# Performance work log

Hardware: AMD Instinct MI355X
Metric: run time of the kernel (lower is better)

## Reference

```python
import jax, jax.numpy as jnp
import numpy as np

EPS = 1e-5
GROUPS = 32
HEADS = 8
RES_SCALE = 0.7071067811865476  # 1/sqrt(2)


def group_norm(x, groups, weight=None, bias=None):
    # x: [b, c, t]; normalize over (c//groups, t) per group, like torch GroupNorm
    b, c, t = x.shape
    xg = x.reshape(b, groups, (c // groups) * t)
    mean = xg.mean(axis=-1, keepdims=True)
    var = xg.var(axis=-1, keepdims=True)
    xg = (xg - mean) * jax.lax.rsqrt(var + EPS)
    x = xg.reshape(b, c, t)
    if weight is not None:
        x = x * weight[None, :, None] + bias[None, :, None]
    return x


def setup_inputs() -> dict:
    key = jax.random.key(0)
    ks = jax.random.split(key, 7)
    b, c, hh, ww = 8, 512, 32, 32
    return {
        "x": jax.random.normal(ks[0], (b, c, hh, ww), dtype=jnp.float32),
        "gn_w": jax.random.uniform(ks[1], (c,), dtype=jnp.float32, minval=0.5, maxval=1.5),
        "gn_b": jax.random.normal(ks[2], (c,), dtype=jnp.float32) * 0.1,
        "qkv_w": jax.random.normal(ks[3], (3 * c, c), dtype=jnp.float32) * (c ** -0.5),
        "qkv_b": jax.random.normal(ks[4], (3 * c,), dtype=jnp.float32) * 0.02,
        "proj_w": jax.random.normal(ks[5], (c, c), dtype=jnp.float32) * 0.02,
        "proj_b": jax.random.normal(ks[6], (c,), dtype=jnp.float32) * 0.02,
    }


def reference(x, gn_w, gn_b, qkv_w, qkv_b, proj_w, proj_b):
    b, c, hh, ww = x.shape
    t = hh * ww
    ch = c // HEADS
    xf = x.reshape(b, c, t)
    xn = group_norm(xf, GROUPS, gn_w, gn_b)
    # 1x1 conv -> GEMM: [b, 3c, t]
    qkv = jnp.einsum('oc,bct->bot', qkv_w, xn) + qkv_b[None, :, None]
    # split order: per head contiguous [q_ch; k_ch; v_ch]
    qkv = qkv.reshape(b * HEADS, 3 * ch, t)
    q, k, v = jnp.split(qkv, 3, axis=1)
    scale = ch ** -0.25
    w = jnp.einsum('bct,bcs->bts', q * scale, k * scale)
    w = jax.nn.softmax(w.astype(jnp.float32), axis=-1).astype(qkv.dtype)
    a = jnp.einsum('bts,bcs->bct', w, v).reshape(b, c, t)
    h = jnp.einsum('oc,bct->bot', proj_w, a) + proj_b[None, :, None]
    out = group_norm(RES_SCALE * xn + h, GROUPS)  # functional group_norm: no affine
    return out.reshape(b, c, hh, ww)
```

## Files before the change

### kernel.cpp

```cpp
#include <hip/hip_runtime.h>


typedef unsigned short u16;
typedef __attribute__((ext_vector_type(8))) short short8v;
typedef __attribute__((ext_vector_type(4))) float float4v;

constexpr int NB = 8, NC = 512, NT = 1024, CPG = 16;
#define EPSV 1e-5f
#define RES_SCALE 0.7071067811865476f
#define QK_SCALE 0.35355339059327376f
#define LOG2E 1.4426950408889634f

static __device__ __forceinline__ u16 f2bf(float f) {
  unsigned int u = __builtin_bit_cast(unsigned int, f);
  u = (u + 0x7fffu + ((u >> 16) & 1u)) >> 16;
  return (u16)u;
}
static __device__ __forceinline__ float exp2_fast(float x) {
  float r;
  asm("v_exp_f32 %0, %1" : "=v"(r) : "v"(x));
  return r;
}

template<bool AFFINE>
__global__ __launch_bounds__(256) void groupnorm_kernel(
    const float* __restrict__ src0, const float* __restrict__ gw,
    const float* __restrict__ gb, float* __restrict__ dst0)
{
  const int tid = threadIdx.x;
  const int b = blockIdx.x >> 5;
  const int g = blockIdx.x & 31;
  const size_t off = ((size_t)(b * NC + g * CPG)) * NT;
  const float* src = src0 + off;
  float* dst = dst0 + off;

  const float4* s4 = (const float4*)src;
  float sum = 0.f, sq = 0.f;
  #pragma unroll 4
  for (int i = tid; i < CPG * NT / 4; i += 256) {
    float4 v = s4[i];
    sum += v.x + v.y + v.z + v.w;
    sq  += v.x * v.x + v.y * v.y + v.z * v.z + v.w * v.w;
  }
  #pragma unroll
  for (int off2 = 32; off2; off2 >>= 1) {
    sum += __shfl_xor(sum, off2);
    sq  += __shfl_xor(sq,  off2);
  }
  __shared__ float rs[4], rq[4], stats[2];
  const int wave = tid >> 6, lane = tid & 63;
  if (lane == 0) { rs[wave] = sum; rq[wave] = sq; }
  __syncthreads();
  if (tid == 0) {
    float S = rs[0] + rs[1] + rs[2] + rs[3];
    float Q = rq[0] + rq[1] + rq[2] + rq[3];
    float mean = S * (1.0f / (CPG * NT));
    float var  = Q * (1.0f / (CPG * NT)) - mean * mean;
    stats[0] = mean;
    stats[1] = rsqrtf(var + EPSV);
  }
  __syncthreads();
  const float mean = stats[0], rstd = stats[1];
  float4* d4 = (float4*)dst;
  #pragma unroll 4
  for (int i = tid; i < CPG * NT / 4; i += 256) {
    float a, c2;
    if (AFFINE) {
      int ch = g * CPG + (i >> 8);
      float wv = gw[ch];
      a  = rstd * wv;
      c2 = gb[ch] - mean * a;
    } else {
      a  = rstd;
      c2 = -mean * rstd;
    }
    float4 v = s4[i];
    v.x = v.x * a + c2; v.y = v.y * a + c2;
    v.z = v.z * a + c2; v.w = v.w * a + c2;
    d4[i] = v;
  }
}

__global__ __launch_bounds__(256) void prep_kernel(
    const float* __restrict__ xnf, u16* __restrict__ xbt,
    const float* __restrict__ qw, const float* __restrict__ pw,
    u16* __restrict__ qwb, u16* __restrict__ pwb)
{
  __shared__ __attribute__((aligned(16))) u16 T[64 * 80];
  const int x = blockIdx.x;
  const int tid = threadIdx.x;
  if (x >= 1024) {
    const int i = (x - 1024) * 256 + tid;
    const float* in; u16* out; int j;
    if (i < 98304) { in = qw; out = qwb; j = i; }
    else           { in = pw; out = pwb; j = i - 98304; }
    const float4 a = *(const float4*)(in + (size_t)j * 8);
    const float4 b = *(const float4*)(in + (size_t)j * 8 + 4);
    short8v o;
    o[0] = (short)f2bf(a.x); o[1] = (short)f2bf(a.y);
    o[2] = (short)f2bf(a.z); o[3] = (short)f2bf(a.w);
    o[4] = (short)f2bf(b.x); o[5] = (short)f2bf(b.y);
    o[6] = (short)f2bf(b.z); o[7] = (short)f2bf(b.w);
    *(short8v*)(out + (size_t)j * 8) = o;
    return;
  }
  const int tt = x & 15, cc = (x >> 4) & 7, b = x >> 7;
  const int c = tid >> 2, tch = (tid & 3) * 16;
  const float* src = xnf + ((size_t)b * NC + cc * 64 + c) * NT + tt * 64 + tch;
  #pragma unroll
  for (int j = 0; j < 4; j++) {
    float4 v = *(const float4*)(src + j * 4);
    T[(tch + j * 4 + 0) * 80 + c] = f2bf(v.x);
    T[(tch + j * 4 + 1) * 80 + c] = f2bf(v.y);
    T[(tch + j * 4 + 2) * 80 + c] = f2bf(v.z);
    T[(tch + j * 4 + 3) * 80 + c] = f2bf(v.w);
  }
  __syncthreads();
  const int t = tid >> 2, cp = (tid & 3) * 2;
  u16* dst = xbt + ((size_t)b * NT + tt * 64 + t) * NC + cc * 64;
  #pragma unroll
  for (int q = 0; q < 2; q++)
    *(short8v*)(dst + (cp + q) * 8) = *(const short8v*)(T + t * 80 + (cp + q) * 8);
}

template<int MODE>
__global__ __launch_bounds__(256) void mfma_gemm_kernel(
    const u16* __restrict__ Wb, const float* __restrict__ bias,
    const u16* __restrict__ Bt, u16* __restrict__ qkT,
    u16* __restrict__ vN, float* __restrict__ outF,
    const float* __restrict__ xnf)
{
  __shared__ __attribute__((aligned(16))) u16 lds[(MODE == 1) ? 17408 : 16384];
  const int tid = threadIdx.x;
  const int w = tid >> 6, l = tid & 63, lr = l & 15, lg = l >> 4;
  const int wm = (w >> 1) * 64, wn = (w & 1) * 64;
  const int bn = blockIdx.x * 128, bm = blockIdx.y * 128, b = blockIdx.z;

  const u16* Ag = Wb + (size_t)bm * 512;
  const u16* Bg = Bt + ((size_t)b * NT + bn) * 512;

  const int srow = w * 16 + (l >> 2);
  const int scg  = (l & 3) ^ ((l >> 3) & 3);
  const u16* ap0 = Ag + (size_t)srow * 512 + scg * 8;
  const u16* bp0 = Bg + (size_t)srow * 512 + scg * 8;
  char* ldsb = (char*)lds;
  char* adst0 = ldsb + w * 1024;

  float4v acc[4][4];
  #pragma unroll
  for (int i = 0; i < 4; i++)
    #pragma unroll
    for (int j = 0; j < 4; j++) acc[i][j] = (float4v){0.f, 0.f, 0.f, 0.f};

  #pragma unroll
  for (int r = 0; r < 2; r++) {
    __builtin_amdgcn_global_load_lds(ap0 + r * 64 * 512, adst0 + r * 4096, 16, 0, 0);
    __builtin_amdgcn_global_load_lds(bp0 + r * 64 * 512, adst0 + 8192 + r * 4096, 16, 0, 0);
  }
  asm volatile("s_waitcnt vmcnt(0)" ::: "memory");
  __builtin_amdgcn_s_barrier();

  for (int ks = 0; ks < 16; ++ks) {
    const int buf = ks & 1;
    if (ks < 15) {
      const size_t k0n = (size_t)(ks + 1) * 32;
      char* an = ldsb + (buf ^ 1) * 16384 + w * 1024;
      #pragma unroll
      for (int r = 0; r < 2; r++) {
        __builtin_amdgcn_global_load_lds(ap0 + k0n + r * 64 * 512, an + r * 4096, 16, 0, 0);
        __builtin_amdgcn_global_load_lds(bp0 + k0n + r * 64 * 512, an + 8192 + r * 4096, 16, 0, 0);
      }
    }
    const u16* au = lds + buf * 8192;
    const u16* bu = au + 4096;
    short8v af[4], bf[4];
    #pragma unroll
    for (int mi = 0; mi < 4; mi++) {
      const int m = wm + mi * 16 + lr;
      af[mi] = *(const short8v*)(au + m * 32 + ((lg ^ ((m >> 1) & 3)) * 8));
    }
    #pragma unroll
    for (int ni = 0; ni < 4; ni++) {
      const int n = wn + ni * 16 + lr;
      bf[ni] = *(const short8v*)(bu + n * 32 + ((lg ^ ((n >> 1) & 3)) * 8));
    }
    #pragma unroll
    for (int mi = 0; mi < 4; mi++)
      #pragma unroll
      for (int ni = 0; ni < 4; ni++)
        acc[mi][ni] = __builtin_amdgcn_mfma_f32_16x16x32_bf16(af[mi], bf[ni], acc[mi][ni], 0, 0, 0);
    if (ks < 15) {
      asm volatile("s_waitcnt vmcnt(0)" ::: "memory");
      __builtin_amdgcn_s_barrier();
    }
  }

  if (MODE == 0) {
    #pragma unroll
    for (int mi = 0; mi < 4; mi++) {
      const int m0 = bm + wm + mi * 16 + lg * 4;
      const int head = m0 / 192;
      const int r0 = m0 - head * 192;
      const float4 bv4 = *(const float4*)(bias + m0);
      if (r0 < 128) {
        const float scl = (r0 < 64) ? QK_SCALE * LOG2E : QK_SCALE;
        const int col = head * 128 + r0;
        #pragma unroll
        for (int ni = 0; ni < 4; ni++) {
          const int t = bn + wn + ni * 16 + lr;
          unsigned int lo = (unsigned)f2bf((acc[mi][ni][0] + bv4.x) * scl) |
                            ((unsigned)f2bf((acc[mi][ni][1] + bv4.y) * scl) << 16);
          unsigned int hi = (unsigned)f2bf((acc[mi][ni][2] + bv4.z) * scl) |
                            ((unsigned)f2bf((acc[mi][ni][3] + bv4.w) * scl) << 16);
          *(uint2*)(qkT + ((size_t)b * NT + t) * 1024 + col) = make_uint2(lo, hi);
        }
      } else {
        const int vc = head * 64 + (r0 - 128);
        #pragma unroll
        for (int ni = 0; ni < 4; ni++) {
          const int t = bn + wn + ni * 16 + lr;
          vN[((size_t)b * NC + vc + 0) * NT + t] = f2bf(acc[mi][ni][0] + bv4.x);
          vN[((size_t)b * NC + vc + 1) * NT + t] = f2bf(acc[mi][ni][1] + bv4.y);
          vN[((size_t)b * NC + vc + 2) * NT + t] = f2bf(acc[mi][ni][2] + bv4.z);
          vN[((size_t)b * NC + vc + 3) * NT + t] = f2bf(acc[mi][ni][3] + bv4.w);
        }
      }
    }
  } else {
    float* Cs = (float*)lds;
    for (int ph = 0; ph < 2; ph++) {
      __syncthreads();
      if ((w >> 1) == ph) {
        #pragma unroll
        for (int mi = 0; mi < 4; mi++)
          #pragma unroll
          for (int ni = 0; ni < 4; ni++) {
            const int rr = mi * 16 + lg * 4;
            const int cc2 = wn + ni * 16 + lr;
            #pragma unroll
            for (int r = 0; r < 4; r++)
              Cs[(rr + r) * 136 + cc2] = acc[mi][ni][r];
          }
      }
      __syncthreads();
      const int mloc = tid >> 2;
      const int m = bm + ph * 64 + mloc;
      const float bv = bias[m];
      const int cb = (tid & 3) * 32;
      const float* cr = Cs + mloc * 136 + cb;
      const float* xr = xnf + ((size_t)b * NC + m) * NT + bn + cb;
      float* yr = outF + ((size_t)b * NC + m) * NT + bn + cb;
      #pragma unroll
      for (int j = 0; j < 8; j++) {
        float4 c4 = *(const float4*)(cr + j * 4);
        float4 x4 = *(const float4*)(xr + j * 4);
        float4 o;
        o.x = c4.x + bv + RES_SCALE * x4.x;
        o.y = c4.y + bv + RES_SCALE * x4.y;
        o.z = c4.z + bv + RES_SCALE * x4.z;
        o.w = c4.w + bv + RES_SCALE * x4.w;
        *(float4*)(yr + j * 4) = o;
      }
    }
  }
}

__global__ __launch_bounds__(256, 4) void attn_mfma_kernel(
    const u16* __restrict__ qkT, const u16* __restrict__ vN, u16* __restrict__ aT)
{
  __shared__ __attribute__((aligned(16))) u16 lds[5 * 4096];
  const int tid = threadIdx.x;
  const int w = tid >> 6, l = tid & 63, lr = l & 15, lg = l >> 4;
  const int L = blockIdx.x;
  const int bh = (L & 7) * 8 + ((L >> 3) & 7);
  const int t0 = (L >> 6) * 64;
  const int b = bh >> 3, h = bh & 7;

  const u16* qbase = qkT + (size_t)b * NT * 1024 + h * 128;
  const u16* kbase = qbase + 64;
  const u16* vbase = vN + ((size_t)b * NC + h * 64) * NT;

  const size_t qrow = (size_t)(t0 + w * 16 + lr) * 1024;
  const short8v qa0 = *(const short8v*)(qbase + qrow + lg * 8);
  const short8v qa1 = *(const short8v*)(qbase + qrow + 32 + lg * 8);

  const int strow = w * 8 + (l >> 3);
  const int scg = (l & 7) ^ (l >> 3);
  const u16* kp0 = kbase + (size_t)strow * 1024 + scg * 8;
  const u16* vp0 = vbase + (size_t)strow * 1024 + scg * 8;
  char* ldsb = (char*)lds;
  u16* Ps = lds + 16384;

  float4v out[4];
  #pragma unroll
  for (int nc = 0; nc < 4; nc++) out[nc] = (float4v){0.f, 0.f, 0.f, 0.f};
  float ps[4] = {0.f, 0.f, 0.f, 0.f};

  #pragma unroll
  for (int r = 0; r < 2; r++) {
    __builtin_amdgcn_global_load_lds(kp0 + (size_t)r * 32 * 1024,
                                     ldsb + w * 1024 + r * 4096, 16, 0, 0);
    __builtin_amdgcn_global_load_lds(vp0 + (size_t)r * 32 * 1024,
                                     ldsb + 16384 + w * 1024 + r * 4096, 16, 0, 0);
  }
  asm volatile("s_waitcnt vmcnt(0)" ::: "memory");
  __builtin_amdgcn_s_barrier();

  for (int it = 0; it < 16; ++it) {
    const int buf = it & 1;
    if (it < 15) {
      const size_t s0n = (size_t)(it + 1) * 64;
      char* kd = ldsb + (buf ^ 1) * 8192 + w * 1024;
      char* vd = ldsb + 16384 + (buf ^ 1) * 8192 + w * 1024;
      #pragma unroll
      for (int r = 0; r < 2; r++) {
        __builtin_amdgcn_global_load_lds(kp0 + (s0n + r * 32) * 1024, kd + r * 4096, 16, 0, 0);
        __builtin_amdgcn_global_load_lds(vp0 + s0n + (size_t)r * 32 * 1024, vd + r * 4096, 16, 0, 0);
      }
    }
    const u16* Kc = lds + buf * 4096;
    const u16* Vc = lds + 8192 + buf * 4096;

    float4v sacc[4];
    #pragma unroll
    for (int n = 0; n < 4; n++) sacc[n] = (float4v){0.f, 0.f, 0.f, 0.f};
    __builtin_amdgcn_s_setprio(1);
    #pragma unroll
    for (int n = 0; n < 4; n++) {
      const int srow = n * 16 + lr;
      short8v kb0 = *(const short8v*)(Kc + srow * 64 + ((lg ^ (srow & 7)) * 8));
      short8v kb1 = *(const short8v*)(Kc + srow * 64 + (((4 + lg) ^ (srow & 7)) * 8));
      sacc[n] = __builtin_amdgcn_mfma_f32_16x16x32_bf16(qa0, kb0, sacc[n], 0, 0, 0);
      sacc[n] = __builtin_amdgcn_mfma_f32_16x16x32_bf16(qa1, kb1, sacc[n], 0, 0, 0);
    }
    __builtin_amdgcn_s_setprio(0);

    #pragma unroll
    for (int n = 0; n < 4; n++) {
      #pragma unroll
      for (int r = 0; r < 4; r++) {
        float p = exp2_fast(sacc[n][r]);
        ps[r] += p;
        const int t = w * 16 + lg * 4 + r;
        Ps[t * 64 + ((n * 16 + lr) ^ ((t & 7) << 3))] =
            (u16)(__builtin_bit_cast(unsigned int, p) >> 16);
      }
    }

    __builtin_amdgcn_s_setprio(1);
    #pragma unroll
    for (int kc = 0; kc < 2; kc++) {
      const int prow = w * 16 + lr;
      short8v pa = *(const short8v*)(Ps + prow * 64 + ((kc * 32 + lg * 8) ^ ((prow & 7) << 3)));
      #pragma unroll
      for (int nc = 0; nc < 4; nc++) {
        const int crow = nc * 16 + lr;
        short8v vb = *(const short8v*)(Vc + crow * 64 + (((kc * 4 + lg) ^ (crow & 7)) * 8));
        out[nc] = __builtin_amdgcn_mfma_f32_16x16x32_bf16(pa, vb, out[nc], 0, 0, 0);
      }
    }
    __builtin_amdgcn_s_setprio(0);

    if (it < 15) {
      asm volatile("s_waitcnt vmcnt(0)" ::: "memory");
      __builtin_amdgcn_s_barrier();
    }
  }

  #pragma unroll
  for (int r = 0; r < 4; r++) {
    ps[r] += __shfl_xor(ps[r], 1);
    ps[r] += __shfl_xor(ps[r], 2);
    ps[r] += __shfl_xor(ps[r], 4);
    ps[r] += __shfl_xor(ps[r], 8);
  }

  __syncthreads();
  u16* At = lds;
  float inv[4];
  #pragma unroll
  for (int r = 0; r < 4; r++) inv[r] = 1.0f / ps[r];
  #pragma unroll
  for (int nc = 0; nc < 4; nc++)
    #pragma unroll
    for (int r = 0; r < 4; r++)
      At[(w * 16 + lg * 4 + r) * 80 + nc * 16 + lr] = f2bf(out[nc][r] * inv[r]);
  __syncthreads();
  const int t = tid >> 2, cp = (tid & 3) * 2;
  u16* dst = aT + ((size_t)b * NT + t0 + t) * NC + h * 64;
  #pragma unroll
  for (int q = 0; q < 2; q++)
    *(short8v*)(dst + (cp + q) * 8) = *(const short8v*)(At + t * 80 + (cp + q) * 8);
}

extern "C" void kernel_launch(void* const* d_in, const int* in_sizes, int n_in,
                              void* d_out, int out_size, void* d_ws, size_t ws_size,
                              hipStream_t stream)
{
  const float* x      = (const float*)d_in[0];
  const float* gn_w   = (const float*)d_in[1];
  const float* gn_b   = (const float*)d_in[2];
  const float* qkv_w  = (const float*)d_in[3];
  const float* qkv_b  = (const float*)d_in[4];
  const float* proj_w = (const float*)d_in[5];
  const float* proj_b = (const float*)d_in[6];
  float* out = (float*)d_out;

  float* xn  = (float*)d_ws;
  u16* base16 = (u16*)(xn + (size_t)NB * NC * NT);
  u16* xbt = base16;
  u16* qkT = xbt + (size_t)NB * NT * NC;
  u16* vN  = qkT + (size_t)NB * NT * 1024;
  u16* aT  = vN + (size_t)NB * NC * NT;
  u16* qwb = aT + (size_t)NB * NT * NC;
  u16* pwb = qwb + 1536 * 512;

  groupnorm_kernel<true><<<dim3(NB * 32), 256, 0, stream>>>(x, gn_w, gn_b, xn);
  prep_kernel<<<dim3(1536), 256, 0, stream>>>(xn, xbt, qkv_w, proj_w, qwb, pwb);
  mfma_gemm_kernel<0><<<dim3(8, 12, NB), 256, 0, stream>>>(qwb, qkv_b, xbt, qkT, vN, nullptr, nullptr);
  attn_mfma_kernel<<<dim3(1024), 256, 0, stream>>>(qkT, vN, aT);
  mfma_gemm_kernel<1><<<dim3(8, 4, NB), 256, 0, stream>>>(pwb, proj_b, aT, nullptr, nullptr, out, xn);
  groupnorm_kernel<false><<<dim3(256), 256, 0, stream>>>(out, nullptr, nullptr, out);
}
```

Before: 167.2 us.

## Fuse first groupnorm into bf16 transpose prep and transpose attention MFMA operands

The first group norm now writes the normalized fp32 activations and the transposed bf16 copy from a single kernel, using an LDS transpose per group. This removes one launch and one full re-read of the normalized tensor. The attention kernel swaps the MFMA operand order so each lane holds one query row. That lets the softmax row sum be reduced with two shuffles instead of sixteen, and lets P and the output be packed with v_cvt_pk_bf16 into wider LDS stores. Risks are a 48KB LDS footprint in the fused prep kernel, which limits occupancy, and LDS bank conflicts on its transpose writes.

```diff
diff --git a/kernel.cpp b/kernel.cpp
--- a/kernel.cpp
+++ b/kernel.cpp
@@ -21,76 +21,24 @@
   asm("v_exp_f32 %0, %1" : "=v"(r) : "v"(x));
   return r;
 }
-
-template<bool AFFINE>
-__global__ __launch_bounds__(256) void groupnorm_kernel(
-    const float* __restrict__ src0, const float* __restrict__ gw,
-    const float* __restrict__ gb, float* __restrict__ dst0)
-{
-  const int tid = threadIdx.x;
-  const int b = blockIdx.x >> 5;
-  const int g = blockIdx.x & 31;
-  const size_t off = ((size_t)(b * NC + g * CPG)) * NT;
-  const float* src = src0 + off;
-  float* dst = dst0 + off;
-
-  const float4* s4 = (const float4*)src;
-  float sum = 0.f, sq = 0.f;
-  #pragma unroll 4
-  for (int i = tid; i < CPG * NT / 4; i += 256) {
-    float4 v = s4[i];
-    sum += v.x + v.y + v.z + v.w;
-    sq  += v.x * v.x + v.y * v.y + v.z * v.z + v.w * v.w;
-  }
-  #pragma unroll
-  for (int off2 = 32; off2; off2 >>= 1) {
-    sum += __shfl_xor(sum, off2);
-    sq  += __shfl_xor(sq,  off2);
-  }
-  __shared__ float rs[4], rq[4], stats[2];
-  const int wave = tid >> 6, lane = tid & 63;
-  if (lane == 0) { rs[wave] = sum; rq[wave] = sq; }
-  __syncthreads();
-  if (tid == 0) {
-    float S = rs[0] + rs[1] + rs[2] + rs[3];
-    float Q = rq[0] + rq[1] + rq[2] + rq[3];
-    float mean = S * (1.0f / (CPG * NT));
-    float var  = Q * (1.0f / (CPG * NT)) - mean * mean;
-    stats[0] = mean;
-    stats[1] = rsqrtf(var + EPSV);
-  }
-  __syncthreads();
-  const float mean = stats[0], rstd = stats[1];
-  float4* d4 = (float4*)dst;
-  #pragma unroll 4
-  for (int i = tid; i < CPG * NT / 4; i += 256) {
-    float a, c2;
-    if (AFFINE) {
-      int ch = g * CPG + (i >> 8);
-      float wv = gw[ch];
-      a  = rstd * wv;
-      c2 = gb[ch] - mean * a;
-    } else {
-      a  = rstd;
-      c2 = -mean * rstd;
-    }
-    float4 v = s4[i];
-    v.x = v.x * a + c2; v.y = v.y * a + c2;
-    v.z = v.z * a + c2; v.w = v.w * a + c2;
-    d4[i] = v;
-  }
-}
-
-__global__ __launch_bounds__(256) void prep_kernel(
-    const float* __restrict__ xnf, u16* __restrict__ xbt,
+static __device__ __forceinline__ unsigned cvt_pk_bf16(float lo, float hi) {
+  unsigned r;
+  asm("v_cvt_pk_bf16_f32 %0, %1, %2" : "=v"(r) : "v"(lo), "v"(hi));
+  return r;
+}
+
+__global__ __launch_bounds__(256) void gn1_prep_kernel(
+    const float* __restrict__ x, const float* __restrict__ gw,
+    const float* __restrict__ gb, float* __restrict__ xn, u16* __restrict__ xbt,
     const float* __restrict__ qw, const float* __restrict__ pw,
     u16* __restrict__ qwb, u16* __restrict__ pwb)
 {
-  __shared__ __attribute__((aligned(16))) u16 T[64 * 80];
-  const int x = blockIdx.x;
+  __shared__ __attribute__((aligned(16))) u16 T[1024 * 24];
+  __shared__ float rs[4], rq[4], stats[2];
+  const int blk = blockIdx.x;
   const int tid = threadIdx.x;
-  if (x >= 1024) {
-    const int i = (x - 1024) * 256 + tid;
+  if (blk >= 256) {
+    const int i = (blk - 256) * 256 + tid;
     const float* in; u16* out; int j;
     if (i < 98304) { in = qw; out = qwb; j = i; }
     else           { in = pw; out = pwb; j = i - 98304; }
@@ -104,23 +52,61 @@
     *(short8v*)(out + (size_t)j * 8) = o;
     return;
   }
-  const int tt = x & 15, cc = (x >> 4) & 7, b = x >> 7;
-  const int c = tid >> 2, tch = (tid & 3) * 16;
-  const float* src = xnf + ((size_t)b * NC + cc * 64 + c) * NT + tt * 64 + tch;
-  #pragma unroll
-  for (int j = 0; j < 4; j++) {
-    float4 v = *(const float4*)(src + j * 4);
-    T[(tch + j * 4 + 0) * 80 + c] = f2bf(v.x);
-    T[(tch + j * 4 + 1) * 80 + c] = f2bf(v.y);
-    T[(tch + j * 4 + 2) * 80 + c] = f2bf(v.z);
-    T[(tch + j * 4 + 3) * 80 + c] = f2bf(v.w);
-  }
-  __syncthreads();
-  const int t = tid >> 2, cp = (tid & 3) * 2;
-  u16* dst = xbt + ((size_t)b * NT + tt * 64 + t) * NC + cc * 64;
-  #pragma unroll
-  for (int q = 0; q < 2; q++)
-    *(short8v*)(dst + (cp + q) * 8) = *(const short8v*)(T + t * 80 + (cp + q) * 8);
+  const int b = blk >> 5, g = blk & 31;
+  const size_t off = ((size_t)(b * NC + g * CPG)) * NT;
+  const float4* s4 = (const float4*)(x + off);
+  float sum = 0.f, sq = 0.f;
+  #pragma unroll 4
+  for (int i = tid; i < CPG * NT / 4; i += 256) {
+    float4 v = s4[i];
+    sum += v.x + v.y + v.z + v.w;
+    sq  += v.x * v.x + v.y * v.y + v.z * v.z + v.w * v.w;
+  }
+  #pragma unroll
+  for (int off2 = 32; off2; off2 >>= 1) {
+    sum += __shfl_xor(sum, off2);
+    sq  += __shfl_xor(sq,  off2);
+  }
+  const int wave = tid >> 6, lane = tid & 63;
+  if (lane == 0) { rs[wave] = sum; rq[wave] = sq; }
+  __syncthreads();
+  if (tid == 0) {
+    float S = rs[0] + rs[1] + rs[2] + rs[3];
+    float Q = rq[0] + rq[1] + rq[2] + rq[3];
+    float mean = S * (1.0f / (CPG * NT));
+    float var  = Q * (1.0f / (CPG * NT)) - mean * mean;
+    stats[0] = mean;
+    stats[1] = rsqrtf(var + EPSV);
+  }
+  __syncthreads();
+  const float mean = stats[0], rstd = stats[1];
+  float4* d4 = (float4*)(xn + off);
+  #pragma unroll 4
+  for (int i = tid; i < CPG * NT / 4; i += 256) {
+    const int ch = i >> 8;
+    const float wv = gw[g * CPG + ch];
+    const float a = rstd * wv;
+    const float c2 = gb[g * CPG + ch] - mean * a;
+    float4 v = s4[i];
+    v.x = v.x * a + c2; v.y = v.y * a + c2;
+    v.z = v.z * a + c2; v.w = v.w * a + c2;
+    d4[i] = v;
+    const int t4 = (i & 255) * 4;
+    T[(t4 + 0) * 24 + ch] = f2bf(v.x);
+    T[(t4 + 1) * 24 + ch] = f2bf(v.y);
+    T[(t4 + 2) * 24 + ch] = f2bf(v.z);
+    T[(t4 + 3) * 24 + ch] = f2bf(v.w);
+  }
+  __syncthreads();
+  #pragma unroll
+  for (int tt = 0; tt < 4; tt++) {
+    const int t = tid + 256 * tt;
+    uint4 lo = *(const uint4*)&T[t * 24];
+    uint4 hi = *(const uint4*)&T[t * 24 + 8];
+    u16* dst = xbt + ((size_t)b * NT + t) * NC + g * CPG;
+    *(uint4*)dst = lo;
+    *(uint4*)(dst + 8) = hi;
+  }
 }
 
 template<int MODE>
@@ -265,6 +251,51 @@
   }
 }
 
+__global__ __launch_bounds__(256) void groupnorm2_kernel(float* __restrict__ dst0)
+{
+  const int tid = threadIdx.x;
+  const int b = blockIdx.x >> 5;
+  const int g = blockIdx.x & 31;
+  const size_t off = ((size_t)(b * NC + g * CPG)) * NT;
+  float* dst = dst0 + off;
+  const float4* s4 = (const float4*)dst;
+  float sum = 0.f, sq = 0.f;
+  #pragma unroll 4
+  for (int i = tid; i < CPG * NT / 4; i += 256) {
+    float4 v = s4[i];
+    sum += v.x + v.y + v.z + v.w;
+    sq  += v.x * v.x + v.y * v.y + v.z * v.z + v.w * v.w;
+  }
+  #pragma unroll
+  for (int off2 = 32; off2; off2 >>= 1) {
+    sum += __shfl_xor(sum, off2);
+    sq  += __shfl_xor(sq,  off2);
+  }
+  __shared__ float rs[4], rq[4], stats[2];
+  const int wave = tid >> 6, lane = tid & 63;
+  if (lane == 0) { rs[wave] = sum; rq[wave] = sq; }
+  __syncthreads();
+  if (tid == 0) {
+    float S = rs[0] + rs[1] + rs[2] + rs[3];
+    float Q = rq[0] + rq[1] + rq[2] + rq[3];
+    float mean = S * (1.0f / (CPG * NT));
+    float var  = Q * (1.0f / (CPG * NT)) - mean * mean;
+    stats[0] = mean;
+    stats[1] = rsqrtf(var + EPSV);
+  }
+  __syncthreads();
+  const float mean = stats[0], rstd = stats[1];
+  float4* d4 = (float4*)dst;
+  #pragma unroll 4
+  for (int i = tid; i < CPG * NT / 4; i += 256) {
+    float4 v = s4[i];
+    const float c2 = -mean * rstd;
+    v.x = v.x * rstd + c2; v.y = v.y * rstd + c2;
+    v.z = v.z * rstd + c2; v.w = v.w * rstd + c2;
+    d4[i] = v;
+  }
+}
+
 __global__ __launch_bounds__(256, 4) void attn_mfma_kernel(
     const u16* __restrict__ qkT, const u16* __restrict__ vN, u16* __restrict__ aT)
 {
@@ -289,12 +320,13 @@
   const u16* kp0 = kbase + (size_t)strow * 1024 + scg * 8;
   const u16* vp0 = vbase + (size_t)strow * 1024 + scg * 8;
   char* ldsb = (char*)lds;
-  u16* Ps = lds + 16384;
+  u16* Psw = lds + 16384 + (w * 16 + lr) * 64;
+  const int sx = (lr & 7) << 3;
 
   float4v out[4];
   #pragma unroll
   for (int nc = 0; nc < 4; nc++) out[nc] = (float4v){0.f, 0.f, 0.f, 0.f};
-  float ps[4] = {0.f, 0.f, 0.f, 0.f};
+  float psum = 0.f;
 
   #pragma unroll
   for (int r = 0; r < 2; r++) {
@@ -330,33 +362,32 @@
       const int srow = n * 16 + lr;
       short8v kb0 = *(const short8v*)(Kc + srow * 64 + ((lg ^ (srow & 7)) * 8));
       short8v kb1 = *(const short8v*)(Kc + srow * 64 + (((4 + lg) ^ (srow & 7)) * 8));
-      sacc[n] = __builtin_amdgcn_mfma_f32_16x16x32_bf16(qa0, kb0, sacc[n], 0, 0, 0);
-      sacc[n] = __builtin_amdgcn_mfma_f32_16x16x32_bf16(qa1, kb1, sacc[n], 0, 0, 0);
+      sacc[n] = __builtin_amdgcn_mfma_f32_16x16x32_bf16(kb0, qa0, sacc[n], 0, 0, 0);
+      sacc[n] = __builtin_amdgcn_mfma_f32_16x16x32_bf16(kb1, qa1, sacc[n], 0, 0, 0);
     }
     __builtin_amdgcn_s_setprio(0);
 
     #pragma unroll
     for (int n = 0; n < 4; n++) {
-      #pragma unroll
-      for (int r = 0; r < 4; r++) {
-        float p = exp2_fast(sacc[n][r]);
-        ps[r] += p;
-        const int t = w * 16 + lg * 4 + r;
-        Ps[t * 64 + ((n * 16 + lr) ^ ((t & 7) << 3))] =
-            (u16)(__builtin_bit_cast(unsigned int, p) >> 16);
-      }
+      float p0 = exp2_fast(sacc[n][0]);
+      float p1 = exp2_fast(sacc[n][1]);
+      float p2 = exp2_fast(sacc[n][2]);
+      float p3 = exp2_fast(sacc[n][3]);
+      psum += (p0 + p1) + (p2 + p3);
+      unsigned w0 = cvt_pk_bf16(p0, p1);
+      unsigned w1 = cvt_pk_bf16(p2, p3);
+      *(uint2*)(Psw + ((n * 16 + lg * 4) ^ sx)) = make_uint2(w0, w1);
     }
 
     __builtin_amdgcn_s_setprio(1);
     #pragma unroll
     for (int kc = 0; kc < 2; kc++) {
-      const int prow = w * 16 + lr;
-      short8v pa = *(const short8v*)(Ps + prow * 64 + ((kc * 32 + lg * 8) ^ ((prow & 7) << 3)));
+      short8v pb = *(const short8v*)(Psw + ((kc * 32 + lg * 8) ^ sx));
       #pragma unroll
       for (int nc = 0; nc < 4; nc++) {
         const int crow = nc * 16 + lr;
         short8v vb = *(const short8v*)(Vc + crow * 64 + (((kc * 4 + lg) ^ (crow & 7)) * 8));
-        out[nc] = __builtin_amdgcn_mfma_f32_16x16x32_bf16(pa, vb, out[nc], 0, 0, 0);
+        out[nc] = __builtin_amdgcn_mfma_f32_16x16x32_bf16(vb, pb, out[nc], 0, 0, 0);
       }
     }
     __builtin_amdgcn_s_setprio(0);
@@ -367,24 +398,18 @@
     }
   }
 
-  #pragma unroll
-  for (int r = 0; r < 4; r++) {
-    ps[r] += __shfl_xor(ps[r], 1);
-    ps[r] += __shfl_xor(ps[r], 2);
-    ps[r] += __shfl_xor(ps[r], 4);
-    ps[r] += __shfl_xor(ps[r], 8);
-  }
+  psum += __shfl_xor(psum, 16);
+  psum += __shfl_xor(psum, 32);
+  const float inv = 1.0f / psum;
 
   __syncthreads();
   u16* At = lds;
-  float inv[4];
-  #pragma unroll
-  for (int r = 0; r < 4; r++) inv[r] = 1.0f / ps[r];
-  #pragma unroll
-  for (int nc = 0; nc < 4; nc++)
-    #pragma unroll
-    for (int r = 0; r < 4; r++)
-      At[(w * 16 + lg * 4 + r) * 80 + nc * 16 + lr] = f2bf(out[nc][r] * inv[r]);
+  #pragma unroll
+  for (int nc = 0; nc < 4; nc++) {
+    unsigned w0 = cvt_pk_bf16(out[nc][0] * inv, out[nc][1] * inv);
+    unsigned w1 = cvt_pk_bf16(out[nc][2] * inv, out[nc][3] * inv);
+    *(uint2*)(At + (w * 16 + lr) * 80 + nc * 16 + lg * 4) = make_uint2(w0, w1);
+  }
   __syncthreads();
   const int t = tid >> 2, cp = (tid & 3) * 2;
   u16* dst = aT + ((size_t)b * NT + t0 + t) * NC + h * 64;
@@ -415,10 +440,10 @@
   u16* qwb = aT + (size_t)NB * NT * NC;
   u16* pwb = qwb + 1536 * 512;
 
-  groupnorm_kernel<true><<<dim3(NB * 32), 256, 0, stream>>>(x, gn_w, gn_b, xn);
-  prep_kernel<<<dim3(1536), 256, 0, stream>>>(xn, xbt, qkv_w, proj_w, qwb, pwb);
+  gn1_prep_kernel<<<dim3(768), 256, 0, stream>>>(x, gn_w, gn_b, xn, xbt,
+                                                 qkv_w, proj_w, qwb, pwb);
   mfma_gemm_kernel<0><<<dim3(8, 12, NB), 256, 0, stream>>>(qwb, qkv_b, xbt, qkT, vN, nullptr, nullptr);
   attn_mfma_kernel<<<dim3(1024), 256, 0, stream>>>(qkT, vN, aT);
   mfma_gemm_kernel<1><<<dim3(8, 4, NB), 256, 0, stream>>>(pwb, proj_b, aT, nullptr, nullptr, out, xn);
-  groupnorm_kernel<false><<<dim3(256), 256, 0, stream>>>(out, nullptr, nullptr, out);
-}
+  groupnorm2_kernel<<<dim3(256), 256, 0, stream>>>(out);
+}
```

Result: faster. 159.9 us (-4.4%).
